# Performance work log

Measured on AMD Instinct MI355X. Metric: run time of the kernel, lower is better.

## Reference

```python
import jax, jax.numpy as jnp
import numpy as np

B, T, F = 512, 256, 24
CF = 64            # cnn_filters
IN = 2 * CF        # LNN input size after second conv
UNITS = 128        # lnn_units
DENSE = 64         # dense_units
ODE_UNFOLDS = 6    # semi-implicit ODE solver unfolds (LiquidNet default)


def _maxpool1d(x):  # [B,C,T] -> [B,C,T//2]
    return jax.lax.reduce_window(x, -jnp.inf, jax.lax.max, (1, 1, 2), (1, 1, 2), 'VALID')


def setup_inputs() -> dict:
    key = jax.random.key(0)
    ks = jax.random.split(key, 16)
    u = lambda k, shape, lo, hi: jax.random.uniform(k, shape, jnp.float32, lo, hi)
    return {
        'x': jax.random.normal(ks[0], (B, T, F), jnp.float32),
        'conv1_w': jax.random.normal(ks[1], (CF, F, 5), jnp.float32) * 0.1,
        'conv1_b': jnp.zeros((CF,), jnp.float32),
        'conv2_w': jax.random.normal(ks[2], (2 * CF, CF, 3), jnp.float32) * 0.1,
        'conv2_b': jnp.zeros((2 * CF,), jnp.float32),
        'input_w': jnp.ones((IN,), jnp.float32),
        'input_b': jnp.zeros((IN,), jnp.float32),
        'sensory_mu': u(ks[3], (IN, UNITS), 0.3, 0.8),
        'sensory_sigma': u(ks[4], (IN, UNITS), 3.0, 8.0),
        'sensory_W': u(ks[5], (IN, UNITS), 0.01, 1.0),
        'sensory_erev': jnp.sign(jax.random.normal(ks[6], (IN, UNITS))).astype(jnp.float32),
        'mu': u(ks[7], (UNITS, UNITS), 0.3, 0.8),
        'sigma': u(ks[8], (UNITS, UNITS), 3.0, 8.0),
        'W': u(ks[9], (UNITS, UNITS), 0.01, 1.0),
        'erev': jnp.sign(jax.random.normal(ks[10], (UNITS, UNITS))).astype(jnp.float32),
        'vleak': u(ks[11], (UNITS,), -0.2, 0.2),
        'gleak': jnp.ones((UNITS,), jnp.float32),
        'cm_t': jnp.full((UNITS,), 0.5, jnp.float32),
        'fc1_w': jax.random.normal(ks[12], (DENSE, UNITS), jnp.float32) * 0.05,
        'fc1_b': jnp.zeros((DENSE,), jnp.float32),
        'fc2_w': jax.random.normal(ks[13], (1, DENSE), jnp.float32) * 0.05,
        'fc2_b': jnp.zeros((1,), jnp.float32),
    }


def _forward(x, conv1_w, conv1_b, conv2_w, conv2_b, input_w, input_b,
             sensory_mu, sensory_sigma, sensory_W, sensory_erev,
             mu, sigma, W, erev, vleak, gleak, cm_t,
             fc1_w, fc1_b, fc2_w, fc2_b):
    # --- CNN feature extractor ---
    h = jnp.transpose(x, (0, 2, 1))                        # [B, F, T]
    dn = ('NCH', 'OIH', 'NCH')
    h = jax.lax.conv_general_dilated(h, conv1_w, (1,), 'SAME', dimension_numbers=dn)
    h = _maxpool1d(jax.nn.relu(h + conv1_b[None, :, None]))
    h = jax.lax.conv_general_dilated(h, conv2_w, (1,), 'SAME', dimension_numbers=dn)
    h = _maxpool1d(jax.nn.relu(h + conv2_b[None, :, None]))  # dropout: eval mode (identity)
    feats = jnp.transpose(h, (0, 2, 1))                    # [B, T/4, IN]
    xs = jnp.transpose(feats, (1, 0, 2))                   # [T', B, IN] for scan

    # --- LiquidNet (LTC) recurrence, semi-implicit ODE solver ---
    def step(v, xt):
        xt = xt * input_w + input_b                        # affine input mapping
        s_act = sensory_W * jax.nn.sigmoid((xt[:, :, None] - sensory_mu) * sensory_sigma)  # [B,IN,U]
        w_num_s = jnp.sum(s_act * sensory_erev, axis=1)    # [B,U]
        w_den_s = jnp.sum(s_act, axis=1)
        for _ in range(ODE_UNFOLDS):
            w_act = W * jax.nn.sigmoid((v[:, :, None] - mu) * sigma)  # [B,U,U]
            w_num = jnp.sum(w_act * erev, axis=1) + w_num_s
            w_den = jnp.sum(w_act, axis=1) + w_den_s
            v = (cm_t * v + gleak * vleak + w_num) / (cm_t + gleak + w_den)
        return v, None

    h0 = jnp.zeros((x.shape[0], UNITS), x.dtype)
    hT, _ = jax.lax.scan(jax.checkpoint(step), h0, xs)

    # --- MLP head ---
    y = jax.nn.relu(hT @ fc1_w.T + fc1_b)
    return y @ fc2_w.T + fc2_b                             # [B, 1]


def reference(x, conv1_w, conv1_b, conv2_w, conv2_b, input_w, input_b,
              sensory_mu, sensory_sigma, sensory_W, sensory_erev,
              mu, sigma, W, erev, vleak, gleak, cm_t,
              fc1_w, fc1_b, fc2_w, fc2_b):
    return _forward(x, conv1_w, conv1_b, conv2_w, conv2_b, input_w, input_b,
                    sensory_mu, sensory_sigma, sensory_W, sensory_erev,
                    mu, sigma, W, erev, vleak, gleak, cm_t,
                    fc1_w, fc1_b, fc2_w, fc2_b)
```

## Files before the change

### kernel.cpp

```cpp
#include <hip/hip_runtime.h>
#include <hip/hip_bf16.h>


#define L2E 1.4426950408889634f

__global__ __launch_bounds__(256)
void prep_kernel(const float* __restrict__ smu, const float* __restrict__ ssig,
                 const float* __restrict__ sW,  const float* __restrict__ serev,
                 const float* __restrict__ mu,  const float* __restrict__ sig,
                 const float* __restrict__ W,   const float* __restrict__ erev,
                 const float* __restrict__ in_w, const float* __restrict__ in_b,
                 float2* __restrict__ R12, float* __restrict__ VT,
                 float4* __restrict__ S4) {
  int idx = blockIdx.x * 256 + threadIdx.x;
  int i = idx >> 7;
  float r1 = sig[idx] * L2E;
  R12[idx] = make_float2(r1, mu[idx] * r1);
  VT[idx]  = W[idx] * erev[idx];
  float ss = ssig[idx] * L2E;
  S4[idx] = make_float4(ss * in_w[i], (smu[idx] - in_b[i]) * ss,
                        sW[idx] * serev[idx], 0.f);
}

__launch_bounds__(512)
__global__ void conv1_kernel(const float* __restrict__ x, const float* __restrict__ w1,
                             const float* __restrict__ b1, float* __restrict__ P1) {
  __shared__ float xs[6240];
  int tid = threadIdx.x, b = blockIdx.x;
  const float* xb = x + (size_t)b * 6144;
  for (int idx = tid; idx < 6144; idx += 512) xs[idx + 48] = xb[idx];
  if (tid < 48) { xs[tid] = 0.f; xs[6192 + tid] = 0.f; }
  __syncthreads();
  int tp = tid & 127, cq = tid >> 7;
  float acc0[16], acc1[16];
#pragma unroll
  for (int n = 0; n < 16; n++) { float bb = b1[cq * 16 + n]; acc0[n] = bb; acc1[n] = bb; }
  for (int cic = 0; cic < 3; cic++) {
    float p[6][8];
#pragma unroll
    for (int r = 0; r < 6; r++) {
      const float* row = &xs[(2 * tp + r) * 24 + cic * 8];
      float4 a = *(const float4*)row;
      float4 c = *(const float4*)(row + 4);
      p[r][0] = a.x; p[r][1] = a.y; p[r][2] = a.z; p[r][3] = a.w;
      p[r][4] = c.x; p[r][5] = c.y; p[r][6] = c.z; p[r][7] = c.w;
    }
#pragma unroll
    for (int n = 0; n < 16; n++) {
      const float* wr = w1 + (cq * 16 + n) * 120 + cic * 40;
#pragma unroll
      for (int c = 0; c < 8; c++) {
#pragma unroll
        for (int kk = 0; kk < 5; kk++) {
          float w = wr[c * 5 + kk];
          acc0[n] = fmaf(p[kk][c],     w, acc0[n]);
          acc1[n] = fmaf(p[kk + 1][c], w, acc1[n]);
        }
      }
    }
  }
  float* pb = P1 + (size_t)b * 8192;
#pragma unroll
  for (int n = 0; n < 16; n++)
    pb[(cq * 16 + n) * 128 + tp] = fmaxf(fmaxf(acc0[n], acc1[n]), 0.f);
}

__launch_bounds__(512)
__global__ void conv2_kernel(const float* __restrict__ P1, const float* __restrict__ w2,
                             const float* __restrict__ b2, float* __restrict__ feats) {
  __shared__ float xs[8450];
  int tid = threadIdx.x, b = blockIdx.x;
  const float* pb = P1 + (size_t)b * 8192;
  for (int idx = tid; idx < 8192; idx += 512) {
    int ci = idx >> 7, t = idx & 127;
    xs[(t + 1) * 65 + ci] = pb[idx];
  }
  if (tid < 65) { xs[tid] = 0.f; xs[129 * 65 + tid] = 0.f; }
  __syncthreads();
  int tp = tid & 63, cq = tid >> 6;
  float acc0[16], acc1[16];
#pragma unroll
  for (int n = 0; n < 16; n++) { float bb = b2[cq * 16 + n]; acc0[n] = bb; acc1[n] = bb; }
  for (int cic = 0; cic < 8; cic++) {
    float p[4][8];
#pragma unroll
    for (int r = 0; r < 4; r++)
#pragma unroll
      for (int c = 0; c < 8; c++)
        p[r][c] = xs[(2 * tp + r) * 65 + cic * 8 + c];
#pragma unroll
    for (int n = 0; n < 16; n++) {
      const float* wr = w2 + (cq * 16 + n) * 192 + cic * 24;
#pragma unroll
      for (int c = 0; c < 8; c++) {
#pragma unroll
        for (int kk = 0; kk < 3; kk++) {
          float w = wr[c * 3 + kk];
          acc0[n] = fmaf(p[kk][c],     w, acc0[n]);
          acc1[n] = fmaf(p[kk + 1][c], w, acc1[n]);
        }
      }
    }
  }
  __syncthreads();
#pragma unroll
  for (int n = 0; n < 16; n += 4) {
    float4 v;
    v.x = fmaxf(fmaxf(acc0[n],     acc1[n]),     0.f);
    v.y = fmaxf(fmaxf(acc0[n + 1], acc1[n + 1]), 0.f);
    v.z = fmaxf(fmaxf(acc0[n + 2], acc1[n + 2]), 0.f);
    v.w = fmaxf(fmaxf(acc0[n + 3], acc1[n + 3]), 0.f);
    *(float4*)&xs[tp * 128 + cq * 16 + n] = v;
  }
  __syncthreads();
  float* fb = feats + (size_t)b * 8192;
  for (int idx = tid; idx < 8192; idx += 512) fb[idx] = xs[idx];
}

__launch_bounds__(1024)
__global__ void lnn_kernel(const float2* __restrict__ R12, const float* __restrict__ VT,
                           const float4* __restrict__ S4,
                           const float* __restrict__ feats,
                           const float* __restrict__ cm_t, const float* __restrict__ gleak,
                           const float* __restrict__ vleak,
                           const float* __restrict__ fc1_w, const float* __restrict__ fc1_b,
                           const float* __restrict__ fc2_w, const float* __restrict__ fc2_b,
                           float* __restrict__ out) {
  __shared__ float2 r12lds[16384];
  __shared__ float4 psum[8][128];
  __shared__ float2 vs2[128];
  __shared__ float2 xt2[128];
  __shared__ float red[2][64];
  int tid = threadIdx.x;
  int j = tid & 127, h = tid >> 7;
  int b0 = blockIdx.x * 2;

  for (int idx = tid; idx < 16384; idx += 1024) r12lds[idx] = R12[idx];

  float vw[16];
#pragma unroll
  for (int n = 0; n < 16; n++) vw[n] = VT[(16 * h + n) * 128 + j];

  float cmj = cm_t[j], glk = gleak[j];
  float gvl = glk * vleak[j], cgl = cmj + glk;
  float vj0 = 0.f, vj1 = 0.f;
  if (tid < 128) vs2[j] = make_float2(0.f, 0.f);
  __syncthreads();

  for (int t = 0; t < 64; t++) {
    if (tid < 128) {
      float a = feats[(size_t)b0 * 8192 + t * 128 + j];
      float b = feats[(size_t)(b0 + 1) * 8192 + t * 128 + j];
      xt2[j] = make_float2(a, b);
    }
    __syncthreads();

    float sn0 = 0.f, sd0 = 0.f, sn1 = 0.f, sd1 = 0.f;
    {
      float n0 = 0.f, d0 = 0.f, n1 = 0.f, d1 = 0.f;
      const float4* sp = S4 + (size_t)(16 * h) * 128 + j;
#pragma unroll 8
      for (int n = 0; n < 16; n++) {
        float4 s = sp[n * 128];
        float2 xv = xt2[16 * h + n];
        float q0 = __builtin_amdgcn_rcpf(1.f + __builtin_amdgcn_exp2f(fmaf(-s.x, xv.x, s.y)));
        n0 = fmaf(s.z, q0, n0); d0 = fmaf(fabsf(s.z), q0, d0);
        float q1 = __builtin_amdgcn_rcpf(1.f + __builtin_amdgcn_exp2f(fmaf(-s.x, xv.y, s.y)));
        n1 = fmaf(s.z, q1, n1); d1 = fmaf(fabsf(s.z), q1, d1);
      }
      psum[h][j] = make_float4(n0, d0, n1, d1);
    }
    __syncthreads();
    if (h == 0) {
      float4 a0 = psum[0][j], a1 = psum[1][j], a2 = psum[2][j], a3 = psum[3][j];
      float4 a4 = psum[4][j], a5 = psum[5][j], a6 = psum[6][j], a7 = psum[7][j];
      sn0 = a0.x + a1.x + a2.x + a3.x + a4.x + a5.x + a6.x + a7.x;
      sd0 = a0.y + a1.y + a2.y + a3.y + a4.y + a5.y + a6.y + a7.y;
      sn1 = a0.z + a1.z + a2.z + a3.z + a4.z + a5.z + a6.z + a7.z;
      sd1 = a0.w + a1.w + a2.w + a3.w + a4.w + a5.w + a6.w + a7.w;
    }
    __syncthreads();

    for (int u = 0; u < 6; u++) {
      float n0 = 0.f, d0 = 0.f, n1 = 0.f, d1 = 0.f;
      const float2* mp = &r12lds[(16 * h) * 128 + j];
#pragma unroll
      for (int n = 0; n < 16; n++) {
        float2 rr = mp[n * 128];
        float2 v2 = vs2[16 * h + n];
        float q0 = __builtin_amdgcn_rcpf(1.f + __builtin_amdgcn_exp2f(fmaf(-rr.x, v2.x, rr.y)));
        n0 = fmaf(vw[n], q0, n0); d0 = fmaf(fabsf(vw[n]), q0, d0);
        float q1 = __builtin_amdgcn_rcpf(1.f + __builtin_amdgcn_exp2f(fmaf(-rr.x, v2.y, rr.y)));
        n1 = fmaf(vw[n], q1, n1); d1 = fmaf(fabsf(vw[n]), q1, d1);
      }
      psum[h][j] = make_float4(n0, d0, n1, d1);
      __syncthreads();
      if (h == 0) {
        float4 a0 = psum[0][j], a1 = psum[1][j], a2 = psum[2][j], a3 = psum[3][j];
        float4 a4 = psum[4][j], a5 = psum[5][j], a6 = psum[6][j], a7 = psum[7][j];
        float wn0 = sn0 + a0.x + a1.x + a2.x + a3.x + a4.x + a5.x + a6.x + a7.x;
        float wd0 = sd0 + a0.y + a1.y + a2.y + a3.y + a4.y + a5.y + a6.y + a7.y;
        float wn1 = sn1 + a0.z + a1.z + a2.z + a3.z + a4.z + a5.z + a6.z + a7.z;
        float wd1 = sd1 + a0.w + a1.w + a2.w + a3.w + a4.w + a5.w + a6.w + a7.w;
        float den0 = cgl + wd0, den1 = cgl + wd1;
        float i0 = __builtin_amdgcn_rcpf(den0); i0 = i0 * fmaf(-den0, i0, 2.f);
        float i1 = __builtin_amdgcn_rcpf(den1); i1 = i1 * fmaf(-den1, i1, 2.f);
        vj0 = (fmaf(cmj, vj0, gvl) + wn0) * i0;
        vj1 = (fmaf(cmj, vj1, gvl) + wn1) * i1;
        vs2[j] = make_float2(vj0, vj1);
      }
      __syncthreads();
    }
  }

  if (tid < 128) {
    int g = tid >> 6, d = tid & 63;
    float acc = fc1_b[d];
    for (int u = 0; u < 128; u++) {
      float2 v2 = vs2[u];
      acc = fmaf(g ? v2.y : v2.x, fc1_w[d * 128 + u], acc);
    }
    red[g][d] = fmaxf(acc, 0.f) * fc2_w[d];
  }
  __syncthreads();
  if (tid < 2) {
    float s = fc2_b[0];
    for (int d = 0; d < 64; d++) s += red[tid][d];
    out[b0 + tid] = s;
  }
}

extern "C" void kernel_launch(void* const* d_in, const int* in_sizes, int n_in,
                              void* d_out, int out_size, void* d_ws, size_t ws_size,
                              hipStream_t stream) {
  (void)in_sizes; (void)n_in; (void)out_size; (void)ws_size;
  char* ws = (char*)d_ws;
  float*  P1   = (float*)(ws);
  float*  feats= (float*)(ws + (16 << 20));
  float2* R12  = (float2*)(ws + 0);
  float*  VT   = (float*)(ws + (128 << 10));
  float4* S4   = (float4*)(ws + (192 << 10));

  conv1_kernel<<<512, 512, 0, stream>>>((const float*)d_in[0],
      (const float*)d_in[1], (const float*)d_in[2], P1);
  conv2_kernel<<<512, 512, 0, stream>>>(P1,
      (const float*)d_in[3], (const float*)d_in[4], feats);
  prep_kernel<<<64, 256, 0, stream>>>(
      (const float*)d_in[7], (const float*)d_in[8],
      (const float*)d_in[9], (const float*)d_in[10],
      (const float*)d_in[11], (const float*)d_in[12],
      (const float*)d_in[13], (const float*)d_in[14],
      (const float*)d_in[5], (const float*)d_in[6],
      R12, VT, S4);
  lnn_kernel<<<256, 1024, 0, stream>>>(R12, VT, S4, feats,
      (const float*)d_in[17], (const float*)d_in[16], (const float*)d_in[15],
      (const float*)d_in[18], (const float*)d_in[19],
      (const float*)d_in[20], (const float*)d_in[21],
      (float*)d_out);
}
```

Baseline: 1.229 ms.

## Process one batch row per LNN block and halve the LDS weight tile

Each LNN block now handles one batch element instead of two, launching 512 blocks instead of 256. The LDS copy of the R12 parameters shrinks to its first half, and the upper four thread groups read their part from global memory. LDS use drops so two blocks can share a CU, which is meant to improve occupancy and latency hiding in the barrier-heavy recurrence. The change also prefetches the next timestep's features into a register and swaps __syncthreads for a raw lgkmcnt-wait-plus-barrier. In exchange, per-element parameter reuse is lost, half the group reads come from global or L2 each unfold, and the hand-written barrier does not wait on outstanding global loads (vmcnt).

```diff
diff --git a/kernel.cpp b/kernel.cpp
--- a/kernel.cpp
+++ b/kernel.cpp
@@ -3,6 +3,8 @@
 
 
 #define L2E 1.4426950408889634f
+
+#define BARRIER_LDS() asm volatile("s_waitcnt lgkmcnt(0)\n\ts_barrier" ::: "memory")
 
 __global__ __launch_bounds__(256)
 void prep_kernel(const float* __restrict__ smu, const float* __restrict__ ssig,
@@ -126,16 +128,16 @@
                            const float* __restrict__ fc1_w, const float* __restrict__ fc1_b,
                            const float* __restrict__ fc2_w, const float* __restrict__ fc2_b,
                            float* __restrict__ out) {
-  __shared__ float2 r12lds[16384];
-  __shared__ float4 psum[8][128];
-  __shared__ float2 vs2[128];
-  __shared__ float2 xt2[128];
-  __shared__ float red[2][64];
+  __shared__ float2 r12lds[8192];
+  __shared__ float2 psum[8][128];
+  __shared__ float vs[128];
+  __shared__ float xt[128];
+  __shared__ float red[64];
   int tid = threadIdx.x;
   int j = tid & 127, h = tid >> 7;
-  int b0 = blockIdx.x * 2;
-
-  for (int idx = tid; idx < 16384; idx += 1024) r12lds[idx] = R12[idx];
+  int bb = blockIdx.x;
+
+  for (int idx = tid; idx < 8192; idx += 1024) r12lds[idx] = R12[idx];
 
   float vw[16];
 #pragma unroll
@@ -143,90 +145,89 @@
 
   float cmj = cm_t[j], glk = gleak[j];
   float gvl = glk * vleak[j], cgl = cmj + glk;
-  float vj0 = 0.f, vj1 = 0.f;
-  if (tid < 128) vs2[j] = make_float2(0.f, 0.f);
-  __syncthreads();
+  float vj = 0.f;
+  if (tid < 128) vs[j] = 0.f;
+  float xn = 0.f;
+  if (tid < 128) xn = feats[(size_t)bb * 8192 + j];
+  BARRIER_LDS();
 
   for (int t = 0; t < 64; t++) {
-    if (tid < 128) {
-      float a = feats[(size_t)b0 * 8192 + t * 128 + j];
-      float b = feats[(size_t)(b0 + 1) * 8192 + t * 128 + j];
-      xt2[j] = make_float2(a, b);
-    }
-    __syncthreads();
-
-    float sn0 = 0.f, sd0 = 0.f, sn1 = 0.f, sd1 = 0.f;
+    if (tid < 128) xt[j] = xn;
+    BARRIER_LDS();
+    if (t < 63 && tid < 128)
+      xn = feats[(size_t)bb * 8192 + (t + 1) * 128 + j];
+
+    float sn = 0.f, sd = 0.f;
     {
-      float n0 = 0.f, d0 = 0.f, n1 = 0.f, d1 = 0.f;
+      float n0 = 0.f, d0 = 0.f;
       const float4* sp = S4 + (size_t)(16 * h) * 128 + j;
 #pragma unroll 8
       for (int n = 0; n < 16; n++) {
         float4 s = sp[n * 128];
-        float2 xv = xt2[16 * h + n];
-        float q0 = __builtin_amdgcn_rcpf(1.f + __builtin_amdgcn_exp2f(fmaf(-s.x, xv.x, s.y)));
-        n0 = fmaf(s.z, q0, n0); d0 = fmaf(fabsf(s.z), q0, d0);
-        float q1 = __builtin_amdgcn_rcpf(1.f + __builtin_amdgcn_exp2f(fmaf(-s.x, xv.y, s.y)));
-        n1 = fmaf(s.z, q1, n1); d1 = fmaf(fabsf(s.z), q1, d1);
-      }
-      psum[h][j] = make_float4(n0, d0, n1, d1);
-    }
-    __syncthreads();
+        float xv = xt[16 * h + n];
+        float q = __builtin_amdgcn_rcpf(1.f + __builtin_amdgcn_exp2f(fmaf(-s.x, xv, s.y)));
+        n0 = fmaf(s.z, q, n0); d0 = fmaf(fabsf(s.z), q, d0);
+      }
+      psum[h][j] = make_float2(n0, d0);
+    }
+    BARRIER_LDS();
     if (h == 0) {
-      float4 a0 = psum[0][j], a1 = psum[1][j], a2 = psum[2][j], a3 = psum[3][j];
-      float4 a4 = psum[4][j], a5 = psum[5][j], a6 = psum[6][j], a7 = psum[7][j];
-      sn0 = a0.x + a1.x + a2.x + a3.x + a4.x + a5.x + a6.x + a7.x;
-      sd0 = a0.y + a1.y + a2.y + a3.y + a4.y + a5.y + a6.y + a7.y;
-      sn1 = a0.z + a1.z + a2.z + a3.z + a4.z + a5.z + a6.z + a7.z;
-      sd1 = a0.w + a1.w + a2.w + a3.w + a4.w + a5.w + a6.w + a7.w;
-    }
-    __syncthreads();
-
+      float2 a0 = psum[0][j], a1 = psum[1][j], a2 = psum[2][j], a3 = psum[3][j];
+      float2 a4 = psum[4][j], a5 = psum[5][j], a6 = psum[6][j], a7 = psum[7][j];
+      sn = a0.x + a1.x + a2.x + a3.x + a4.x + a5.x + a6.x + a7.x;
+      sd = a0.y + a1.y + a2.y + a3.y + a4.y + a5.y + a6.y + a7.y;
+    }
+    BARRIER_LDS();
+
+#pragma unroll 1
     for (int u = 0; u < 6; u++) {
-      float n0 = 0.f, d0 = 0.f, n1 = 0.f, d1 = 0.f;
-      const float2* mp = &r12lds[(16 * h) * 128 + j];
-#pragma unroll
-      for (int n = 0; n < 16; n++) {
-        float2 rr = mp[n * 128];
-        float2 v2 = vs2[16 * h + n];
-        float q0 = __builtin_amdgcn_rcpf(1.f + __builtin_amdgcn_exp2f(fmaf(-rr.x, v2.x, rr.y)));
-        n0 = fmaf(vw[n], q0, n0); d0 = fmaf(fabsf(vw[n]), q0, d0);
-        float q1 = __builtin_amdgcn_rcpf(1.f + __builtin_amdgcn_exp2f(fmaf(-rr.x, v2.y, rr.y)));
-        n1 = fmaf(vw[n], q1, n1); d1 = fmaf(fabsf(vw[n]), q1, d1);
-      }
-      psum[h][j] = make_float4(n0, d0, n1, d1);
-      __syncthreads();
+      float n0 = 0.f, d0 = 0.f;
+      if (h < 4) {
+        const float2* mp = &r12lds[(16 * h) * 128 + j];
+#pragma unroll
+        for (int n = 0; n < 16; n++) {
+          float2 rr = mp[n * 128];
+          float v2 = vs[16 * h + n];
+          float q = __builtin_amdgcn_rcpf(1.f + __builtin_amdgcn_exp2f(fmaf(-rr.x, v2, rr.y)));
+          n0 = fmaf(vw[n], q, n0); d0 = fmaf(fabsf(vw[n]), q, d0);
+        }
+      } else {
+        const float2* gp = R12 + (size_t)(16 * h) * 128 + j;
+#pragma unroll 8
+        for (int n = 0; n < 16; n++) {
+          float2 rr = gp[n * 128];
+          float v2 = vs[16 * h + n];
+          float q = __builtin_amdgcn_rcpf(1.f + __builtin_amdgcn_exp2f(fmaf(-rr.x, v2, rr.y)));
+          n0 = fmaf(vw[n], q, n0); d0 = fmaf(fabsf(vw[n]), q, d0);
+        }
+      }
+      psum[h][j] = make_float2(n0, d0);
+      BARRIER_LDS();
       if (h == 0) {
-        float4 a0 = psum[0][j], a1 = psum[1][j], a2 = psum[2][j], a3 = psum[3][j];
-        float4 a4 = psum[4][j], a5 = psum[5][j], a6 = psum[6][j], a7 = psum[7][j];
-        float wn0 = sn0 + a0.x + a1.x + a2.x + a3.x + a4.x + a5.x + a6.x + a7.x;
-        float wd0 = sd0 + a0.y + a1.y + a2.y + a3.y + a4.y + a5.y + a6.y + a7.y;
-        float wn1 = sn1 + a0.z + a1.z + a2.z + a3.z + a4.z + a5.z + a6.z + a7.z;
-        float wd1 = sd1 + a0.w + a1.w + a2.w + a3.w + a4.w + a5.w + a6.w + a7.w;
-        float den0 = cgl + wd0, den1 = cgl + wd1;
-        float i0 = __builtin_amdgcn_rcpf(den0); i0 = i0 * fmaf(-den0, i0, 2.f);
-        float i1 = __builtin_amdgcn_rcpf(den1); i1 = i1 * fmaf(-den1, i1, 2.f);
-        vj0 = (fmaf(cmj, vj0, gvl) + wn0) * i0;
-        vj1 = (fmaf(cmj, vj1, gvl) + wn1) * i1;
-        vs2[j] = make_float2(vj0, vj1);
-      }
-      __syncthreads();
-    }
-  }
-
-  if (tid < 128) {
-    int g = tid >> 6, d = tid & 63;
-    float acc = fc1_b[d];
-    for (int u = 0; u < 128; u++) {
-      float2 v2 = vs2[u];
-      acc = fmaf(g ? v2.y : v2.x, fc1_w[d * 128 + u], acc);
-    }
-    red[g][d] = fmaxf(acc, 0.f) * fc2_w[d];
-  }
-  __syncthreads();
-  if (tid < 2) {
+        float2 a0 = psum[0][j], a1 = psum[1][j], a2 = psum[2][j], a3 = psum[3][j];
+        float2 a4 = psum[4][j], a5 = psum[5][j], a6 = psum[6][j], a7 = psum[7][j];
+        float wn = sn + a0.x + a1.x + a2.x + a3.x + a4.x + a5.x + a6.x + a7.x;
+        float wd = sd + a0.y + a1.y + a2.y + a3.y + a4.y + a5.y + a6.y + a7.y;
+        float den = cgl + wd;
+        float iv = __builtin_amdgcn_rcpf(den); iv = iv * fmaf(-den, iv, 2.f);
+        vj = (fmaf(cmj, vj, gvl) + wn) * iv;
+        vs[j] = vj;
+      }
+      BARRIER_LDS();
+    }
+  }
+
+  if (tid < 64) {
+    float acc = fc1_b[tid];
+    for (int u = 0; u < 128; u++)
+      acc = fmaf(vs[u], fc1_w[tid * 128 + u], acc);
+    red[tid] = fmaxf(acc, 0.f) * fc2_w[tid];
+  }
+  BARRIER_LDS();
+  if (tid == 0) {
     float s = fc2_b[0];
-    for (int d = 0; d < 64; d++) s += red[tid][d];
-    out[b0 + tid] = s;
+    for (int d = 0; d < 64; d++) s += red[d];
+    out[bb] = s;
   }
 }
 
@@ -252,7 +253,7 @@
       (const float*)d_in[13], (const float*)d_in[14],
       (const float*)d_in[5], (const float*)d_in[6],
       R12, VT, S4);
-  lnn_kernel<<<256, 1024, 0, stream>>>(R12, VT, S4, feats,
+  lnn_kernel<<<512, 1024, 0, stream>>>(R12, VT, S4, feats,
       (const float*)d_in[17], (const float*)d_in[16], (const float*)d_in[15],
       (const float*)d_in[18], (const float*)d_in[19],
       (const float*)d_in[20], (const float*)d_in[21],
```

Result: slower. 1.683 ms (+37.0%).
